# Kernel optimization log

Hardware: AMD Instinct MI355X
Metric: run time of the kernel (lower is better)

## Reference

```python
import jax, jax.numpy as jnp
import numpy as np

EPS = 1e-5
SEQ = 64

def ln(x, g, b):
    m = jnp.mean(x, axis=-1, keepdims=True)
    v = jnp.var(x, axis=-1, keepdims=True)
    return (x - m) / jnp.sqrt(v + EPS) * g + b

def gelu(x):
    return jax.nn.gelu(x, approximate=False)  # torch nn.GELU default = exact erf

def setup_inputs() -> dict:
    key = jax.random.key(0)
    ks = jax.random.split(key, 24)
    B, D = 512, 128
    DSGU = 4 * D          # 512
    DATTN = DSGU // 2     # 256
    DEXP = 4 * D          # 512 (tiny-attn expanded dim)
    TF = SEQ * D          # 8192
    H = int(1.1 * TF)     # 9011
    w = lambda k, s: jax.random.normal(k, s, dtype=jnp.float32) * 0.02
    return {
        "x": jax.random.normal(ks[0], (B, SEQ, D), dtype=jnp.float32),
        # TinyAttentionBlock
        "qkv_ln_g": jnp.ones((D,), jnp.float32), "qkv_ln_b": jnp.zeros((D,), jnp.float32),
        "qkv_w": w(ks[1], (D, 3 * DEXP)), "qkv_b": jnp.zeros((3 * DEXP,), jnp.float32),
        "attn_proj_w": w(ks[2], (DEXP, DATTN)), "attn_proj_b": jnp.zeros((DATTN,), jnp.float32),
        "attn_ln_g": jnp.ones((DATTN,), jnp.float32), "attn_ln_b": jnp.zeros((DATTN,), jnp.float32),
        "rel_bias": w(ks[3], (2 * SEQ - 1,)),
        "scale": jnp.asarray(1.0 / np.sqrt(D), jnp.float32),
        # SGU proj_in / proj_spatial / proj_out
        "pin_ln_g": jnp.ones((D,), jnp.float32), "pin_ln_b": jnp.zeros((D,), jnp.float32),
        "pin_w": w(ks[4], (D, DSGU)), "pin_b": jnp.zeros((DSGU,), jnp.float32),
        "sp_ln_g": jnp.ones((SEQ,), jnp.float32), "sp_ln_b": jnp.zeros((SEQ,), jnp.float32),
        "sp_w": w(ks[5], (SEQ, SEQ)), "sp_b": jnp.ones((SEQ,), jnp.float32),  # bias init 1.0 per source
        "pout_ln_g": jnp.ones((DATTN,), jnp.float32), "pout_ln_b": jnp.zeros((DATTN,), jnp.float32),
        "pout_w": w(ks[6], (DATTN, D)), "pout_b": jnp.zeros((D,), jnp.float32),
        # ResidualBlock MLP
        "mlp_ln_g": jnp.ones((TF,), jnp.float32), "mlp_ln_b": jnp.zeros((TF,), jnp.float32),
        "mlp_w1": w(ks[7], (TF, H)), "mlp_b1": jnp.zeros((H,), jnp.float32),
        "mlp_w2": w(ks[8], (H, TF)), "mlp_b2": jnp.zeros((TF,), jnp.float32),
    }

def reference(x, qkv_ln_g, qkv_ln_b, qkv_w, qkv_b, attn_proj_w, attn_proj_b,
              attn_ln_g, attn_ln_b, rel_bias, scale,
              pin_ln_g, pin_ln_b, pin_w, pin_b, sp_ln_g, sp_ln_b, sp_w, sp_b,
              pout_ln_g, pout_ln_b, pout_w, pout_b,
              mlp_ln_g, mlp_ln_b, mlp_w1, mlp_b1, mlp_w2, mlp_b2):
    B = x.shape[0]
    # --- TinyAttentionBlock ---
    h = ln(x, qkv_ln_g, qkv_ln_b) @ qkv_w + qkv_b          # [B,64,3*512]
    q, k, v = jnp.split(h, 3, axis=-1)                      # each [B,64,512]
    idx = jnp.arange(SEQ)
    rel = idx[None, :] - idx[:, None] + (SEQ - 1)           # [64,64] in [0,126]
    bias = rel_bias[rel]                                    # [64,64]
    attn = jnp.einsum('bnd,bmd->bnm', q, k) + bias
    attn = jax.nn.softmax(attn, axis=-1) * scale            # post-softmax scale (as in source)
    av = jnp.einsum('bnm,bmd->bnd', attn, v)                # [B,64,512]
    a = ln(av @ attn_proj_w + attn_proj_b, attn_ln_g, attn_ln_b)  # [B,64,256]
    # --- SpatialGatingUnit ---
    h2 = gelu(ln(x, pin_ln_g, pin_ln_b) @ pin_w + pin_b)    # [B,64,512]
    u, vv = jnp.split(h2, 2, axis=-1)                        # [B,64,256] each
    vt = jnp.swapaxes(vv, 1, 2)                              # [B,256,64]
    vt = gelu(ln(vt, sp_ln_g, sp_ln_b) @ sp_w + sp_b)        # spatial proj over seq dim
    vv = jnp.swapaxes(vt, 1, 2)                              # [B,64,256]
    out = u * (vv + a)
    out = ln(out, pout_ln_g, pout_ln_b) @ pout_w + pout_b    # [B,64,128]
    x = x + out
    # --- ResidualBlock MLP on flattened board ---
    xf = x.reshape(B, -1)                                    # [B,8192]
    h3 = gelu(ln(xf, mlp_ln_g, mlp_ln_b) @ mlp_w1 + mlp_b1)  # [B,9011]
    xf = xf + (h3 @ mlp_w2 + mlp_b2)
    return xf.reshape(B, SEQ, -1)
```

## Files before the change

kernel.cpp:

```cpp
#include <hip/hip_runtime.h>
#include <hip/hip_bf16.h>
#include <math.h>

typedef float f32x4 __attribute__((ext_vector_type(4)));
typedef float f32x2 __attribute__((ext_vector_type(2)));
typedef short s16x8 __attribute__((ext_vector_type(8)));
typedef short s16x4 __attribute__((ext_vector_type(4)));
typedef int   i32x4 __attribute__((ext_vector_type(4)));

__device__ __forceinline__ short f2bf(float f) {
  __hip_bfloat16 h = __float2bfloat16(f);
  return __builtin_bit_cast(short, h);
}
__device__ __forceinline__ float bf2f(short s) {
  __hip_bfloat16 h = __builtin_bit_cast(__hip_bfloat16, s);
  return __bfloat162float(h);
}
__device__ __forceinline__ float gelu_f(float x) {
  return 0.5f * x * (1.f + erff(x * 0.70710678118654752440f));
}
__device__ __forceinline__ float waveSum(float v) {
  #pragma unroll
  for (int d = 32; d; d >>= 1) v += __shfl_xor(v, d);
  return v;
}

__global__ __launch_bounds__(256) void ln_dual_k(
    const float* __restrict__ x,
    const float* __restrict__ qg, const float* __restrict__ qb,
    const float* __restrict__ pg, const float* __restrict__ pb,
    short* __restrict__ lnq, short* __restrict__ lnp)
{
  int w = threadIdx.x >> 6, lane = threadIdx.x & 63;
  size_t row = (size_t)blockIdx.x * 4 + w;
  f32x2 v = reinterpret_cast<const f32x2*>(x + row * 128)[lane];
  float s  = v[0] + v[1];
  float sq = v[0]*v[0] + v[1]*v[1];
  s = waveSum(s); sq = waveSum(sq);
  float m = s * (1.f/128.f);
  float rstd = rsqrtf(sq * (1.f/128.f) - m*m + 1e-5f);
  int c = lane * 2;
  float a0 = (v[0]-m)*rstd, a1 = (v[1]-m)*rstd;
  unsigned q0 = (unsigned short)f2bf(a0*qg[c] + qb[c]);
  unsigned q1 = (unsigned short)f2bf(a1*qg[c+1] + qb[c+1]);
  unsigned p0 = (unsigned short)f2bf(a0*pg[c] + pb[c]);
  unsigned p1 = (unsigned short)f2bf(a1*pg[c+1] + pb[c+1]);
  ((unsigned*)lnq)[row*64 + lane] = q0 | (q1 << 16);
  ((unsigned*)lnp)[row*64 + lane] = p0 | (p1 << 16);
}

__global__ __launch_bounds__(256) void ln256_k(
    const float* __restrict__ in,
    const float* __restrict__ g, const float* __restrict__ bb,
    float* __restrict__ out)
{
  int w = threadIdx.x >> 6, lane = threadIdx.x & 63;
  size_t row = (size_t)blockIdx.x * 4 + w;
  f32x4 v = reinterpret_cast<const f32x4*>(in + row * 256)[lane];
  float s  = v[0]+v[1]+v[2]+v[3];
  float sq = v[0]*v[0]+v[1]*v[1]+v[2]*v[2]+v[3]*v[3];
  s = waveSum(s); sq = waveSum(sq);
  float m = s * (1.f/256.f);
  float rstd = rsqrtf(sq * (1.f/256.f) - m*m + 1e-5f);
  f32x4 g4 = reinterpret_cast<const f32x4*>(g)[lane];
  f32x4 b4 = reinterpret_cast<const f32x4*>(bb)[lane];
  f32x4 o;
  #pragma unroll
  for (int k = 0; k < 4; ++k) o[k] = (v[k]-m)*rstd*g4[k] + b4[k];
  reinterpret_cast<f32x4*>(out + row * 256)[lane] = o;
}

__global__ __launch_bounds__(256) void ln8192_k(
    const float* __restrict__ x1,
    const float* __restrict__ g, const float* __restrict__ bb,
    short* __restrict__ lnx)
{
  __shared__ float red[8];
  int t = threadIdx.x, w = t >> 6, lane = t & 63;
  int b = blockIdx.x;
  const f32x4* xr = reinterpret_cast<const f32x4*>(x1 + (size_t)b * 8192);
  f32x4 vals[8];
  float s = 0.f, sq = 0.f;
  #pragma unroll
  for (int i = 0; i < 8; ++i) {
    f32x4 v = xr[t + i*256];
    vals[i] = v;
    s  += v[0]+v[1]+v[2]+v[3];
    sq += v[0]*v[0]+v[1]*v[1]+v[2]*v[2]+v[3]*v[3];
  }
  s = waveSum(s); sq = waveSum(sq);
  if (lane == 0) { red[w] = s; red[4+w] = sq; }
  __syncthreads();
  s  = red[0]+red[1]+red[2]+red[3];
  sq = red[4]+red[5]+red[6]+red[7];
  float m = s * (1.f/8192.f);
  float rstd = rsqrtf(sq * (1.f/8192.f) - m*m + 1e-5f);
  #pragma unroll
  for (int i = 0; i < 8; ++i) {
    int idx = (t + i*256) * 4;
    f32x4 g4 = reinterpret_cast<const f32x4*>(g)[t + i*256];
    f32x4 b4 = reinterpret_cast<const f32x4*>(bb)[t + i*256];
    s16x4 o;
    #pragma unroll
    for (int k = 0; k < 4; ++k) o[k] = f2bf((vals[i][k]-m)*rstd*g4[k] + b4[k]);
    *reinterpret_cast<s16x4*>(&lnx[(size_t)b*8192 + idx]) = o;
  }
}

template<int BM, int BN, int WM, int WN, int EPI>
__global__ __launch_bounds__(256) void gemm_k(
    const short* __restrict__ A, const float* __restrict__ Bw,
    const float* __restrict__ bias, const float* __restrict__ res,
    void* __restrict__ O0, void* __restrict__ O1,
    int M, int N, int K, int Nreal, int Kreal)
{
  constexpr int BK = 64;
  __shared__ __align__(16) short As[BM][BK + 8];
  __shared__ __align__(16) short Bs[BN][BK + 8];
  const int t = threadIdx.x;
  const int lane = t & 63;
  const int w = t >> 6;
  const int wm = w / WN, wn = w % WN;
  const int ln15 = lane & 15, hi = lane >> 4;
  const int m0 = blockIdx.y * BM;
  const int n0 = blockIdx.x * BN;

  f32x4 acc[4][4] = {};

  for (int k0 = 0; k0 < K; k0 += BK) {
    #pragma unroll
    for (int i = 0; i < (BM*BK)/(256*8); ++i) {
      int e = (i*256 + t) * 8;
      int r = e / BK, c = e % BK;
      *reinterpret_cast<i32x4*>(&As[r][c]) =
          *reinterpret_cast<const i32x4*>(&A[(size_t)(m0 + r) * K + k0 + c]);
    }
    #pragma unroll
    for (int i = 0; i < (BK*BN)/256; ++i) {
      int idx = i*256 + t;
      int n = idx % BN, k = idx / BN;
      int gk = k0 + k, gn = n0 + n;
      float v = (gk < Kreal && gn < Nreal) ? Bw[(size_t)gk * Nreal + gn] : 0.f;
      Bs[n][k] = f2bf(v);
    }
    __syncthreads();
    #pragma unroll
    for (int kk = 0; kk < BK; kk += 32) {
      s16x8 af[4], bfr[4];
      #pragma unroll
      for (int fm = 0; fm < 4; ++fm)
        af[fm] = *reinterpret_cast<const s16x8*>(&As[wm*64 + fm*16 + ln15][kk + hi*8]);
      #pragma unroll
      for (int fn = 0; fn < 4; ++fn)
        bfr[fn] = *reinterpret_cast<const s16x8*>(&Bs[wn*64 + fn*16 + ln15][kk + hi*8]);
      #pragma unroll
      for (int fm = 0; fm < 4; ++fm)
        #pragma unroll
        for (int fn = 0; fn < 4; ++fn)
          acc[fm][fn] = __builtin_amdgcn_mfma_f32_16x16x32_bf16(
              af[fm], bfr[fn], acc[fm][fn], 0, 0, 0);
    }
    __syncthreads();
  }

  #pragma unroll
  for (int fm = 0; fm < 4; ++fm) {
    #pragma unroll
    for (int fn = 0; fn < 4; ++fn) {
      #pragma unroll
      for (int j = 0; j < 4; ++j) {
        int row = m0 + wm*64 + fm*16 + hi*4 + j;
        int col = n0 + wn*64 + fn*16 + ln15;
        float v = acc[fm][fn][j];
        if constexpr (EPI == 0) {
          v += bias[col];
          ((short*)O0)[(size_t)row * N + col] = f2bf(v);
        } else if constexpr (EPI == 1) {
          v += bias[col];
          ((float*)O0)[(size_t)row * N + col] = v;
        } else if constexpr (EPI == 2) {
          v = gelu_f(v + bias[col]);
          if (col < 256) ((float*)O0)[(size_t)row * 256 + col] = v;
          else ((short*)O1)[(size_t)row * 256 + (col - 256)] = f2bf(v);
        } else {
          v += bias[col] + res[(size_t)row * N + col];
          ((float*)O0)[(size_t)row * N + col] = v;
        }
      }
    }
  }
}

__global__ __launch_bounds__(512, 2) void gemm_splitk3(
    const short* __restrict__ A, const float* __restrict__ Bw,
    float* __restrict__ part,
    int N, int K, int Kreal, int ldb, int kchunk, int ntiles)
{
  __shared__ __align__(16) short As[512 * 64];
  __shared__ __align__(16) short Bs[128 * 72];
  const int t = threadIdx.x, lane = t & 63, w = t >> 6;
  const int ln15 = lane & 15, hi = lane >> 4;
  const int nt = blockIdx.x % ntiles, z = blockIdx.x / ntiles;
  const int n0 = nt * 128;
  const int kbeg = z * kchunk;
  const int kend = (kbeg + kchunk < K) ? (kbeg + kchunk) : K;
  const int nsteps = (kend - kbeg) >> 6;

  const int arow = t >> 3, ag = t & 7;
  const int agsw = ag ^ (arow & 7);
  const int bn = t & 127;
  const int bk0 = (t >> 7) * 16;
  const bool bcol_ok = (n0 + bn) < ldb;

  i32x4 ar[8];
  float br[16];

  auto loadAB = [&](int k0) {
    #pragma unroll
    for (int i = 0; i < 8; ++i)
      ar[i] = *reinterpret_cast<const i32x4*>(
          &A[(size_t)(arow + 64 * i) * K + k0 + ag * 8]);
    const float* bp = Bw + (size_t)(k0 + bk0) * ldb + n0 + bn;
    #pragma unroll
    for (int m = 0; m < 16; ++m) {
      int gk = k0 + bk0 + m;
      br[m] = (bcol_ok && gk < Kreal) ? bp[(size_t)m * ldb] : 0.f;
    }
  };
  auto writeAB = [&]() {
    #pragma unroll
    for (int i = 0; i < 8; ++i) {
      int rr = arow + 64 * i;
      *reinterpret_cast<i32x4*>(&As[rr * 64 + agsw * 8]) = ar[i];
    }
    s16x8 v0, v1;
    #pragma unroll
    for (int m = 0; m < 8; ++m) { v0[m] = f2bf(br[m]); v1[m] = f2bf(br[8 + m]); }
    *reinterpret_cast<s16x8*>(&Bs[bn * 72 + bk0]) = v0;
    *reinterpret_cast<s16x8*>(&Bs[bn * 72 + bk0 + 8]) = v1;
  };

  f32x4 acc[4][8] = {};

  loadAB(kbeg);
  writeAB();
  __syncthreads();

  for (int s = 0; s < nsteps; ++s) {
    if (s + 1 < nsteps) loadAB(kbeg + (s + 1) * 64);
    #pragma unroll
    for (int kk = 0; kk < 2; ++kk) {
      int g = kk * 4 + hi;
      s16x8 af[4];
      #pragma unroll
      for (int fm = 0; fm < 4; ++fm) {
        int row = w * 64 + fm * 16 + ln15;
        af[fm] = *reinterpret_cast<const s16x8*>(&As[row * 64 + ((g ^ (row & 7)) * 8)]);
      }
      #pragma unroll
      for (int fn = 0; fn < 8; ++fn) {
        s16x8 bv = *reinterpret_cast<const s16x8*>(&Bs[(fn * 16 + ln15) * 72 + g * 8]);
        #pragma unroll
        for (int fm = 0; fm < 4; ++fm)
          acc[fm][fn] = __builtin_amdgcn_mfma_f32_16x16x32_bf16(
              af[fm], bv, acc[fm][fn], 0, 0, 0);
      }
    }
    __syncthreads();
    if (s + 1 < nsteps) { writeAB(); __syncthreads(); }
  }

  #pragma unroll
  for (int fm = 0; fm < 4; ++fm)
    #pragma unroll
    for (int fn = 0; fn < 8; ++fn)
      #pragma unroll
      for (int j = 0; j < 4; ++j) {
        int row = w * 64 + fm * 16 + hi * 4 + j;
        int col = n0 + fn * 16 + ln15;
        part[((size_t)z * 512 + row) * N + col] = acc[fm][fn][j];
      }
}

__global__ __launch_bounds__(256) void reduce_mlp1_k(
    const float* __restrict__ part, const float* __restrict__ bias,
    short* __restrict__ h3, int N, int Nreal, int M)
{
  int col4 = (blockIdx.x * 256 + threadIdx.x) * 4;
  int row = blockIdx.y;
  if (col4 >= N) return;
  size_t base = (size_t)row * N + col4;
  size_t stride = (size_t)M * N;
  f32x4 s = *reinterpret_cast<const f32x4*>(part + base);
  #pragma unroll
  for (int ks = 1; ks < 4; ++ks)
    s += *reinterpret_cast<const f32x4*>(part + base + (size_t)ks * stride);
  s16x4 o;
  #pragma unroll
  for (int j = 0; j < 4; ++j) {
    int c = col4 + j;
    float v = 0.f;
    if (c < Nreal) v = gelu_f(s[j] + bias[c]);
    o[j] = f2bf(v);
  }
  *reinterpret_cast<s16x4*>(h3 + base) = o;
}

__global__ __launch_bounds__(256) void reduce_mlp2_k(
    const float* __restrict__ part, const float* __restrict__ bias,
    const float* __restrict__ x1, float* __restrict__ out, int N, int M)
{
  int col4 = (blockIdx.x * 256 + threadIdx.x) * 4;
  int row = blockIdx.y;
  size_t base = (size_t)row * N + col4;
  size_t stride = (size_t)M * N;
  f32x4 s = *reinterpret_cast<const f32x4*>(part + base);
  #pragma unroll
  for (int ks = 1; ks < 4; ++ks)
    s += *reinterpret_cast<const f32x4*>(part + base + (size_t)ks * stride);
  f32x4 b4 = *reinterpret_cast<const f32x4*>(bias + col4);
  f32x4 r4 = *reinterpret_cast<const f32x4*>(x1 + base);
  #pragma unroll
  for (int j = 0; j < 4; ++j) s[j] += b4[j] + r4[j];
  *reinterpret_cast<f32x4*>(out + base) = s;
}

__global__ __launch_bounds__(256) void attn_k(
    const short* __restrict__ qkv, const float* __restrict__ relb,
    const float* __restrict__ scale_p, short* __restrict__ av)
{
  __shared__ __align__(16) short qlds[64][136];
  __shared__ __align__(16) short klds[64][136];
  __shared__ __align__(16) short plds[64][72];
  __shared__ __align__(16) short vlds[128][72];
  __shared__ float rb[127];
  int t = threadIdx.x, lane = t & 63, w = t >> 6;
  int ln15 = lane & 15, hi = lane >> 4;
  int b = blockIdx.x;
  if (t < 127) rb[t] = relb[t];

  f32x4 sacc[4] = {};
  for (int kc = 0; kc < 4; ++kc) {
    #pragma unroll
    for (int i = 0; i < 4; ++i) {
      int e = (i*256 + t) * 8;
      int r = e >> 7, c = e & 127;
      size_t base = (size_t)(b*64 + r) * 1536 + kc*128 + c;
      *reinterpret_cast<i32x4*>(&qlds[r][c]) = *reinterpret_cast<const i32x4*>(&qkv[base]);
      *reinterpret_cast<i32x4*>(&klds[r][c]) = *reinterpret_cast<const i32x4*>(&qkv[base + 512]);
    }
    __syncthreads();
    #pragma unroll
    for (int kk = 0; kk < 128; kk += 32) {
      s16x8 aq = *reinterpret_cast<const s16x8*>(&qlds[16*w + ln15][kk + hi*8]);
      #pragma unroll
      for (int fn = 0; fn < 4; ++fn) {
        s16x8 bk = *reinterpret_cast<const s16x8*>(&klds[fn*16 + ln15][kk + hi*8]);
        sacc[fn] = __builtin_amdgcn_mfma_f32_16x16x32_bf16(aq, bk, sacc[fn], 0, 0, 0);
      }
    }
    __syncthreads();
  }

  float scale = scale_p[0];
  #pragma unroll
  for (int j = 0; j < 4; ++j) {
    int row = 16*w + hi*4 + j;
    float pv[4];
    float mx = -1e30f;
    #pragma unroll
    for (int fn = 0; fn < 4; ++fn) {
      int col = fn*16 + ln15;
      pv[fn] = sacc[fn][j] + rb[col - row + 63];
      mx = fmaxf(mx, pv[fn]);
    }
    #pragma unroll
    for (int d = 1; d < 16; d <<= 1) mx = fmaxf(mx, __shfl_xor(mx, d));
    float sum = 0.f;
    #pragma unroll
    for (int fn = 0; fn < 4; ++fn) { pv[fn] = __expf(pv[fn] - mx); sum += pv[fn]; }
    #pragma unroll
    for (int d = 1; d < 16; d <<= 1) sum += __shfl_xor(sum, d);
    float inv = scale / sum;
    #pragma unroll
    for (int fn = 0; fn < 4; ++fn) plds[row][fn*16 + ln15] = f2bf(pv[fn] * inv);
  }
  __syncthreads();

  for (int cc = 0; cc < 4; ++cc) {
    #pragma unroll
    for (int i = 0; i < 8; ++i) {
      int idx = i*256 + t;
      int s = idx >> 5, c4 = (idx & 31) * 4;
      s16x4 vw = *reinterpret_cast<const s16x4*>(
          &qkv[(size_t)(b*64 + s) * 1536 + 1024 + cc*128 + c4]);
      vlds[c4+0][s] = vw[0]; vlds[c4+1][s] = vw[1];
      vlds[c4+2][s] = vw[2]; vlds[c4+3][s] = vw[3];
    }
    __syncthreads();
    f32x4 pacc[8] = {};
    #pragma unroll
    for (int kk = 0; kk < 64; kk += 32) {
      s16x8 ap = *reinterpret_cast<const s16x8*>(&plds[16*w + ln15][kk + hi*8]);
      #pragma unroll
      for (int fn = 0; fn < 8; ++fn) {
        s16x8 bv = *reinterpret_cast<const s16x8*>(&vlds[fn*16 + ln15][kk + hi*8]);
        pacc[fn] = __builtin_amdgcn_mfma_f32_16x16x32_bf16(ap, bv, pacc[fn], 0, 0, 0);
      }
    }
    #pragma unroll
    for (int fn = 0; fn < 8; ++fn)
      #pragma unroll
      for (int j = 0; j < 4; ++j) {
        int row = b*64 + 16*w + hi*4 + j;
        int col = cc*128 + fn*16 + ln15;
        av[(size_t)row * 512 + col] = f2bf(pacc[fn][j]);
      }
    __syncthreads();
  }
}

__global__ __launch_bounds__(256) void gate_k(
    const float* __restrict__ u, const short* __restrict__ vbf,
    const float* __restrict__ a,
    const float* __restrict__ spg_g, const float* __restrict__ spg_b,
    const float* __restrict__ spw, const float* __restrict__ spb,
    const float* __restrict__ pog, const float* __restrict__ pob,
    short* __restrict__ outn)
{
  __shared__ __align__(16) short nvb[256][72];
  __shared__ __align__(16) short spwT[64][72];
  __shared__ float s_spg[64], s_spbl[64], s_spb[64];
  __shared__ float s_pog[256], s_pob[256];
  int t = threadIdx.x, lane = t & 63, w = t >> 6;
  int ln15 = lane & 15, hi = lane >> 4;
  int b = blockIdx.x;

  if (t < 64) { s_spg[t] = spg_g[t]; s_spbl[t] = spg_b[t]; s_spb[t] = spb[t]; }
  s_pog[t] = pog[t]; s_pob[t] = pob[t];
  #pragma unroll
  for (int i = 0; i < 16; ++i) {
    int idx = i*256 + t;
    int sr = idx >> 6, tc = idx & 63;
    spwT[tc][sr] = f2bf(spw[idx]);
  }

  float vvv[64];
  {
    int c = t;
    float s = 0.f, sq = 0.f;
    #pragma unroll
    for (int si = 0; si < 64; ++si) {
      float f = bf2f(vbf[(size_t)(b*64 + si) * 256 + c]);
      vvv[si] = f; s += f; sq += f*f;
    }
    float m = s * (1.f/64.f);
    float rstd = rsqrtf(sq * (1.f/64.f) - m*m + 1e-5f);
    __syncthreads();
    #pragma unroll
    for (int si = 0; si < 64; ++si)
      nvb[c][si] = f2bf((vvv[si]-m)*rstd*s_spg[si] + s_spbl[si]);
  }
  __syncthreads();

  f32x4 yacc[4][4] = {};
  #pragma unroll
  for (int kk = 0; kk < 64; kk += 32) {
    s16x8 af[4], bfr[4];
    #pragma unroll
    for (int fm = 0; fm < 4; ++fm)
      af[fm] = *reinterpret_cast<const s16x8*>(&nvb[64*w + fm*16 + ln15][kk + hi*8]);
    #pragma unroll
    for (int fn = 0; fn < 4; ++fn)
      bfr[fn] = *reinterpret_cast<const s16x8*>(&spwT[fn*16 + ln15][kk + hi*8]);
    #pragma unroll
    for (int fm = 0; fm < 4; ++fm)
      #pragma unroll
      for (int fn = 0; fn < 4; ++fn)
        yacc[fm][fn] = __builtin_amdgcn_mfma_f32_16x16x32_bf16(
            af[fm], bfr[fn], yacc[fm][fn], 0, 0, 0);
  }
  __syncthreads();

  short (*outl)[264] = reinterpret_cast<short(*)[264]>(&nvb[0][0]);
  #pragma unroll
  for (int fm = 0; fm < 4; ++fm) {
    #pragma unroll
    for (int fn = 0; fn < 4; ++fn) {
      int crow = 64*w + fm*16 + hi*4;
      int tcol = fn*16 + ln15;
      f32x4 u4 = *reinterpret_cast<const f32x4*>(&u[(size_t)(b*64 + tcol)*256 + crow]);
      f32x4 a4 = *reinterpret_cast<const f32x4*>(&a[(size_t)(b*64 + tcol)*256 + crow]);
      #pragma unroll
      for (int j = 0; j < 4; ++j) {
        float g = gelu_f(yacc[fm][fn][j] + s_spb[tcol]);
        float o = u4[j] * (g + a4[j]);
        outl[tcol][crow + j] = f2bf(o);
      }
    }
  }
  __syncthreads();

  #pragma unroll
  for (int ri = 0; ri < 16; ++ri) {
    int trow = w*16 + ri;
    int c = lane * 4;
    s16x4 raw = *reinterpret_cast<const s16x4*>(&outl[trow][c]);
    float f0 = bf2f(raw[0]), f1 = bf2f(raw[1]), f2 = bf2f(raw[2]), f3 = bf2f(raw[3]);
    float s  = f0+f1+f2+f3;
    float sq = f0*f0+f1*f1+f2*f2+f3*f3;
    s = waveSum(s); sq = waveSum(sq);
    float m = s * (1.f/256.f);
    float rstd = rsqrtf(sq * (1.f/256.f) - m*m + 1e-5f);
    s16x4 o;
    o[0] = f2bf((f0-m)*rstd*s_pog[c+0] + s_pob[c+0]);
    o[1] = f2bf((f1-m)*rstd*s_pog[c+1] + s_pob[c+1]);
    o[2] = f2bf((f2-m)*rstd*s_pog[c+2] + s_pob[c+2]);
    o[3] = f2bf((f3-m)*rstd*s_pog[c+3] + s_pob[c+3]);
    *reinterpret_cast<s16x4*>(&outn[(size_t)(b*64 + trow)*256 + c]) = o;
  }
}

extern "C" void kernel_launch(void* const* d_in, const int* in_sizes, int n_in,
                              void* d_out, int out_size, void* d_ws, size_t ws_size,
                              hipStream_t stream)
{
  const float* x          = (const float*)d_in[0];
  const float* qkv_ln_g   = (const float*)d_in[1];
  const float* qkv_ln_b   = (const float*)d_in[2];
  const float* qkv_w      = (const float*)d_in[3];
  const float* qkv_b      = (const float*)d_in[4];
  const float* attn_pw    = (const float*)d_in[5];
  const float* attn_pb    = (const float*)d_in[6];
  const float* attn_ln_g  = (const float*)d_in[7];
  const float* attn_ln_b  = (const float*)d_in[8];
  const float* rel_bias   = (const float*)d_in[9];
  const float* scale      = (const float*)d_in[10];
  const float* pin_ln_g   = (const float*)d_in[11];
  const float* pin_ln_b   = (const float*)d_in[12];
  const float* pin_w      = (const float*)d_in[13];
  const float* pin_b      = (const float*)d_in[14];
  const float* sp_ln_g    = (const float*)d_in[15];
  const float* sp_ln_b    = (const float*)d_in[16];
  const float* sp_w       = (const float*)d_in[17];
  const float* sp_b       = (const float*)d_in[18];
  const float* pout_ln_g  = (const float*)d_in[19];
  const float* pout_ln_b  = (const float*)d_in[20];
  const float* pout_w     = (const float*)d_in[21];
  const float* pout_b     = (const float*)d_in[22];
  const float* mlp_ln_g   = (const float*)d_in[23];
  const float* mlp_ln_b   = (const float*)d_in[24];
  const float* mlp_w1     = (const float*)d_in[25];
  const float* mlp_b1     = (const float*)d_in[26];
  const float* mlp_w2     = (const float*)d_in[27];
  const float* mlp_b2     = (const float*)d_in[28];

  char* ws = (char*)d_ws;
  short* lnq  = (short*)(ws + 0);
  short* lnp  = (short*)(ws + 8388608);
  short* qkvb = (short*)(ws + 16777216);
  short* avb  = (short*)(ws + 117440512);
  float* projb= (float*)(ws + 16777216);
  float* ab   = (float*)(ws + 50331648);
  float* ub   = (float*)(ws + 83886080);
  short* vbfb = (short*)(ws + 117440512);
  short* outnb= (short*)(ws + 134217728);
  float* x1b  = (float*)(ws + 0);
  short* lnxb = (short*)(ws + 150994944);
  short* h3b  = (short*)(ws + 159383552);
  float* partb= (float*)(ws + 16777216);

  ln_dual_k<<<8192, 256, 0, stream>>>(x, qkv_ln_g, qkv_ln_b, pin_ln_g, pin_ln_b, lnq, lnp);
  gemm_k<128,128,2,2,0><<<dim3(12,256), 256, 0, stream>>>(
      lnq, qkv_w, qkv_b, nullptr, qkvb, nullptr, 32768, 1536, 128, 1536, 128);
  attn_k<<<512, 256, 0, stream>>>(qkvb, rel_bias, scale, avb);
  gemm_k<128,128,2,2,1><<<dim3(2,256), 256, 0, stream>>>(
      avb, attn_pw, attn_pb, nullptr, projb, nullptr, 32768, 256, 512, 256, 512);
  ln256_k<<<8192, 256, 0, stream>>>(projb, attn_ln_g, attn_ln_b, ab);
  gemm_k<128,128,2,2,2><<<dim3(4,256), 256, 0, stream>>>(
      lnp, pin_w, pin_b, nullptr, ub, vbfb, 32768, 512, 128, 512, 128);
  gate_k<<<512, 256, 0, stream>>>(ub, vbfb, ab, sp_ln_g, sp_ln_b, sp_w, sp_b,
                                  pout_ln_g, pout_ln_b, outnb);
  gemm_k<128,128,2,2,3><<<dim3(1,256), 256, 0, stream>>>(
      outnb, pout_w, pout_b, x, x1b, nullptr, 32768, 128, 256, 128, 256);
  ln8192_k<<<512, 256, 0, stream>>>(x1b, mlp_ln_g, mlp_ln_b, lnxb);

  gemm_splitk3<<<284, 512, 0, stream>>>(
      lnxb, mlp_w1, partb, 9088, 8192, 8192,
      9011, 2048, 71);
  reduce_mlp1_k<<<dim3(9, 512), 256, 0, stream>>>(partb, mlp_b1, h3b, 9088, 9011, 512);

  gemm_splitk3<<<256, 512, 0, stream>>>(
      h3b, mlp_w2, partb, 8192, 9088, 9011,
      8192, 2304, 64);
  reduce_mlp2_k<<<dim3(8, 512), 256, 0, stream>>>(partb, mlp_b2, x1b, (float*)d_out, 8192, 512);
}
```

Baseline: 803.0 us.

## Load A fragments directly from global and double-buffer B in split-K GEMM

The split-K MLP GEMM no longer stages A tiles in LDS. Each wave loads its own bf16 A fragments straight from global memory, since no other wave in the block reuses those rows. B moves to a double-buffered, XOR-swizzled LDS layout, which cuts the barriers to one per k-step. The first MLP GEMM also drops from 4 to 3 K-splits, and the reduce kernels take the split count as a parameter. The risk is exposed global-load latency for A, because those loads are issued only shortly before the MFMAs that consume them.

```diff
diff --git a/kernel.cpp b/kernel.cpp
--- a/kernel.cpp
+++ b/kernel.cpp
@@ -191,13 +191,12 @@
   }
 }
 
-__global__ __launch_bounds__(512, 2) void gemm_splitk3(
+__global__ __launch_bounds__(512, 2) void gemm_splitk5(
     const short* __restrict__ A, const float* __restrict__ Bw,
     float* __restrict__ part,
     int N, int K, int Kreal, int ldb, int kchunk, int ntiles)
 {
-  __shared__ __align__(16) short As[512 * 64];
-  __shared__ __align__(16) short Bs[128 * 72];
+  __shared__ __align__(16) short Bs[2][128 * 64];
   const int t = threadIdx.x, lane = t & 63, w = t >> 6;
   const int ln15 = lane & 15, hi = lane >> 4;
   const int nt = blockIdx.x % ntiles, z = blockIdx.x / ntiles;
@@ -206,68 +205,65 @@
   const int kend = (kbeg + kchunk < K) ? (kbeg + kchunk) : K;
   const int nsteps = (kend - kbeg) >> 6;
 
-  const int arow = t >> 3, ag = t & 7;
-  const int agsw = ag ^ (arow & 7);
   const int bn = t & 127;
-  const int bk0 = (t >> 7) * 16;
-  const bool bcol_ok = (n0 + bn) < ldb;
-
-  i32x4 ar[8];
+  const int bg0 = (t >> 7) * 2;
+  const bool bok = (n0 + bn) < ldb;
+  const int bsw = bn & 7;
+
   float br[16];
-
-  auto loadAB = [&](int k0) {
-    #pragma unroll
-    for (int i = 0; i < 8; ++i)
-      ar[i] = *reinterpret_cast<const i32x4*>(
-          &A[(size_t)(arow + 64 * i) * K + k0 + ag * 8]);
-    const float* bp = Bw + (size_t)(k0 + bk0) * ldb + n0 + bn;
+  auto loadB = [&](int k0) {
+    const float* bp = Bw + (size_t)(k0 + bg0 * 8) * ldb + n0 + bn;
     #pragma unroll
     for (int m = 0; m < 16; ++m) {
-      int gk = k0 + bk0 + m;
-      br[m] = (bcol_ok && gk < Kreal) ? bp[(size_t)m * ldb] : 0.f;
+      int gk = k0 + bg0 * 8 + m;
+      br[m] = (bok && gk < Kreal) ? bp[(size_t)m * ldb] : 0.f;
     }
   };
-  auto writeAB = [&]() {
-    #pragma unroll
-    for (int i = 0; i < 8; ++i) {
-      int rr = arow + 64 * i;
-      *reinterpret_cast<i32x4*>(&As[rr * 64 + agsw * 8]) = ar[i];
-    }
+  auto writeB = [&](int buf) {
     s16x8 v0, v1;
     #pragma unroll
     for (int m = 0; m < 8; ++m) { v0[m] = f2bf(br[m]); v1[m] = f2bf(br[8 + m]); }
-    *reinterpret_cast<s16x8*>(&Bs[bn * 72 + bk0]) = v0;
-    *reinterpret_cast<s16x8*>(&Bs[bn * 72 + bk0 + 8]) = v1;
+    short* dst = &Bs[buf][bn * 64];
+    *reinterpret_cast<s16x8*>(dst + ((bg0    ) ^ bsw) * 8) = v0;
+    *reinterpret_cast<s16x8*>(dst + ((bg0 + 1) ^ bsw) * 8) = v1;
   };
 
   f32x4 acc[4][8] = {};
 
-  loadAB(kbeg);
-  writeAB();
+  loadB(kbeg);
+  writeB(0);
   __syncthreads();
 
   for (int s = 0; s < nsteps; ++s) {
-    if (s + 1 < nsteps) loadAB(kbeg + (s + 1) * 64);
-    #pragma unroll
-    for (int kk = 0; kk < 2; ++kk) {
-      int g = kk * 4 + hi;
-      s16x8 af[4];
+    const int k0 = kbeg + s * 64;
+    s16x8 af[8];
+    #pragma unroll
+    for (int kk = 0; kk < 2; ++kk)
       #pragma unroll
       for (int fm = 0; fm < 4; ++fm) {
         int row = w * 64 + fm * 16 + ln15;
-        af[fm] = *reinterpret_cast<const s16x8*>(&As[row * 64 + ((g ^ (row & 7)) * 8)]);
-      }
+        af[kk * 4 + fm] = *reinterpret_cast<const s16x8*>(
+            &A[(size_t)row * K + k0 + (kk * 4 + hi) * 8]);
+      }
+    if (s + 1 < nsteps) loadB(k0 + 64);
+
+    const short* bsrc = &Bs[s & 1][0];
+    #pragma unroll
+    for (int kk = 0; kk < 2; ++kk) {
+      const int g = kk * 4 + hi;
       #pragma unroll
       for (int fn = 0; fn < 8; ++fn) {
-        s16x8 bv = *reinterpret_cast<const s16x8*>(&Bs[(fn * 16 + ln15) * 72 + g * 8]);
+        int row = fn * 16 + ln15;
+        s16x8 bv = *reinterpret_cast<const s16x8*>(
+            &bsrc[row * 64 + ((g ^ (row & 7)) * 8)]);
         #pragma unroll
         for (int fm = 0; fm < 4; ++fm)
           acc[fm][fn] = __builtin_amdgcn_mfma_f32_16x16x32_bf16(
-              af[fm], bv, acc[fm][fn], 0, 0, 0);
-      }
-    }
-    __syncthreads();
-    if (s + 1 < nsteps) { writeAB(); __syncthreads(); }
+              af[kk * 4 + fm], bv, acc[fm][fn], 0, 0, 0);
+      }
+    }
+    if (s + 1 < nsteps) writeB((s + 1) & 1);
+    __syncthreads();
   }
 
   #pragma unroll
@@ -284,7 +280,7 @@
 
 __global__ __launch_bounds__(256) void reduce_mlp1_k(
     const float* __restrict__ part, const float* __restrict__ bias,
-    short* __restrict__ h3, int N, int Nreal, int M)
+    short* __restrict__ h3, int N, int Nreal, int M, int ks)
 {
   int col4 = (blockIdx.x * 256 + threadIdx.x) * 4;
   int row = blockIdx.y;
@@ -292,9 +288,8 @@
   size_t base = (size_t)row * N + col4;
   size_t stride = (size_t)M * N;
   f32x4 s = *reinterpret_cast<const f32x4*>(part + base);
-  #pragma unroll
-  for (int ks = 1; ks < 4; ++ks)
-    s += *reinterpret_cast<const f32x4*>(part + base + (size_t)ks * stride);
+  for (int k = 1; k < ks; ++k)
+    s += *reinterpret_cast<const f32x4*>(part + base + (size_t)k * stride);
   s16x4 o;
   #pragma unroll
   for (int j = 0; j < 4; ++j) {
@@ -308,16 +303,15 @@
 
 __global__ __launch_bounds__(256) void reduce_mlp2_k(
     const float* __restrict__ part, const float* __restrict__ bias,
-    const float* __restrict__ x1, float* __restrict__ out, int N, int M)
+    const float* __restrict__ x1, float* __restrict__ out, int N, int M, int ks)
 {
   int col4 = (blockIdx.x * 256 + threadIdx.x) * 4;
   int row = blockIdx.y;
   size_t base = (size_t)row * N + col4;
   size_t stride = (size_t)M * N;
   f32x4 s = *reinterpret_cast<const f32x4*>(part + base);
-  #pragma unroll
-  for (int ks = 1; ks < 4; ++ks)
-    s += *reinterpret_cast<const f32x4*>(part + base + (size_t)ks * stride);
+  for (int k = 1; k < ks; ++k)
+    s += *reinterpret_cast<const f32x4*>(part + base + (size_t)k * stride);
   f32x4 b4 = *reinterpret_cast<const f32x4*>(bias + col4);
   f32x4 r4 = *reinterpret_cast<const f32x4*>(x1 + base);
   #pragma unroll
@@ -585,13 +579,13 @@
       outnb, pout_w, pout_b, x, x1b, nullptr, 32768, 128, 256, 128, 256);
   ln8192_k<<<512, 256, 0, stream>>>(x1b, mlp_ln_g, mlp_ln_b, lnxb);
 
-  gemm_splitk3<<<284, 512, 0, stream>>>(
+  gemm_splitk5<<<213, 512, 0, stream>>>(
       lnxb, mlp_w1, partb, 9088, 8192, 8192,
-      9011, 2048, 71);
-  reduce_mlp1_k<<<dim3(9, 512), 256, 0, stream>>>(partb, mlp_b1, h3b, 9088, 9011, 512);
-
-  gemm_splitk3<<<256, 512, 0, stream>>>(
+      9011, 2752, 71);
+  reduce_mlp1_k<<<dim3(9, 512), 256, 0, stream>>>(partb, mlp_b1, h3b, 9088, 9011, 512, 3);
+
+  gemm_splitk5<<<256, 512, 0, stream>>>(
       h3b, mlp_w2, partb, 8192, 9088, 9011,
       8192, 2304, 64);
-  reduce_mlp2_k<<<dim3(8, 512), 256, 0, stream>>>(partb, mlp_b2, x1b, (float*)d_out, 8192, 512);
-}
+  reduce_mlp2_k<<<dim3(8, 512), 256, 0, stream>>>(partb, mlp_b2, x1b, (float*)d_out, 8192, 512, 4);
+}
```

Result: no change. 792.7 us (-1.3%).
